# Performance work log

Measured on AMD Instinct MI355X. Metric: run time of the kernel, lower is better.

The kernel has to match this reference:

```python
import jax, jax.numpy as jnp
import numpy as np


def setup_inputs() -> dict:
    key = jax.random.key(0)
    k1, k2, k3, k4 = jax.random.split(key, 4)
    B, C, T, H, W = 2, 64, 8, 48, 48
    C2 = C // 2
    x_in = jax.random.normal(k1, (B, C, T, H, W), dtype=jnp.float32)
    # per-time-slice 1x1 conv weights (theta/phi pairs), kaiming-ish scale
    theta_w = jax.random.normal(k2, (T, C2, C), dtype=jnp.float32) / np.sqrt(C)
    phi_w = jax.random.normal(k3, (T, C2, C), dtype=jnp.float32) / np.sqrt(C)
    out_w = jax.random.normal(k4, (C, C), dtype=jnp.float32) / np.sqrt(C)
    return {"x_in": x_in, "theta_w": theta_w, "phi_w": phi_w, "out_w": out_w}


def reference(x_in, theta_w, phi_w, out_w):
    B, C, T, H, W = x_in.shape
    C2 = theta_w.shape[1]
    P = H * W
    # [B, T, C, P] layout: flatten spatial, move time next to batch
    x = jnp.transpose(x_in, (0, 2, 1, 3, 4)).reshape(B, T, C, P)
    # per-slice 1x1 convs == per-slice channel matmuls with slice-specific weights
    theta = jnp.einsum("toc,btcp->btop", theta_w, x)  # [B,T,C2,P]
    phi = jnp.einsum("toc,btcp->btop", phi_w, x)      # [B,T,C2,P]
    scale = 1.0 / jnp.sqrt(jnp.asarray(C2, dtype=x_in.dtype))
    scores = jnp.einsum("btcp,btcq->btpq", theta, phi) * scale  # [B,T,P,P]
    attn = jax.nn.softmax(scores, axis=-1)
    f = jnp.einsum("btpq,btcq->btcp", attn, x)  # value = raw x, [B,T,C,P]
    # conv_out: 1x1x1 Conv3d (pointwise over channels), then residual
    out = jnp.einsum("oc,btcp->btop", out_w, f)
    out = jnp.transpose(out.reshape(B, T, C, H, W), (0, 2, 1, 3, 4))
    return out + x_in
```

## Files before the change

kernel.cpp:

```cpp
#include <hip/hip_runtime.h>
#include <hip/hip_bf16.h>

#define CC 64
#define TT 8
#define PP 2304
#define C2 32
#define BT 16
#define NKT 36
#define SCALE2 0.25503486f

using h8 = __attribute__((ext_vector_type(8))) _Float16;
using h4 = __attribute__((ext_vector_type(4))) _Float16;
using f4 = __attribute__((ext_vector_type(4))) float;

#if __has_builtin(__builtin_amdgcn_exp2f)
#define EXP2(v) __builtin_amdgcn_exp2f(v)
#else
#define EXP2(v) exp2f(v)
#endif

#define SWIZ_BT(xcd, g) ((xcd) + 8 * ((g) & 1))


__global__ __launch_bounds__(256) void k_prep(
    const float* __restrict__ x, const float* __restrict__ tw,
    const float* __restrict__ pw, _Float16* __restrict__ thf,
    _Float16* __restrict__ rec) {
  const int bt = SWIZ_BT(blockIdx.x, blockIdx.y);
  const int qt = blockIdx.y >> 2;
  const int g = (blockIdx.y >> 1) & 1;
  const int b = bt >> 3, t = bt & 7;
  const int tid = threadIdx.x;
  const int wv = tid >> 6, lane = tid & 63;
  const int quad = lane >> 4, l15 = lane & 15;

  __shared__ __align__(16) float x_s[32][68];
  __shared__ __align__(16) _Float16 th_s[2][16][32];
  __shared__ __align__(16) _Float16 ph_s[2][16][32];

  const size_t xslice = ((size_t)b * CC * TT + t) * PP;
  const int qg0 = qt * 64 + g * 32;
  _Float16* rb = rec + (size_t)(bt * NKT + qt) * 6144;
  const f4 zero = {0.f, 0.f, 0.f, 0.f};

  {
    const int qoff = (tid & 7) * 4;
    const int c0 = tid >> 3;
#pragma unroll
    for (int ppass = 0; ppass < 2; ppass++) {
      const int c = ppass * 32 + c0;
      float4 u = *reinterpret_cast<const float4*>(
          &x[xslice + (size_t)c * (TT * PP) + qg0 + qoff]);
      x_s[qoff + 0][c] = u.x;
      x_s[qoff + 1][c] = u.y;
      x_s[qoff + 2][c] = u.z;
      x_s[qoff + 3][c] = u.w;
    }
  }
  __syncthreads();

  if (wv < 2) {
    h8 bx[2];
#pragma unroll
    for (int ks = 0; ks < 2; ks++) {
      const float* row = &x_s[wv * 16 + l15][ks * 32 + quad * 8];
      float4 u0 = *reinterpret_cast<const float4*>(row);
      float4 u1 = *reinterpret_cast<const float4*>(row + 4);
      bx[ks][0] = (_Float16)u0.x; bx[ks][1] = (_Float16)u0.y;
      bx[ks][2] = (_Float16)u0.z; bx[ks][3] = (_Float16)u0.w;
      bx[ks][4] = (_Float16)u1.x; bx[ks][5] = (_Float16)u1.y;
      bx[ks][6] = (_Float16)u1.z; bx[ks][7] = (_Float16)u1.w;
    }

    const float* twt = tw + t * C2 * CC;
    const float* pwt = pw + t * C2 * CC;
    f4 accT[2] = {zero, zero}, accP[2] = {zero, zero};
#pragma unroll
    for (int mt = 0; mt < 2; mt++)
#pragma unroll
      for (int ks = 0; ks < 2; ks++) {
        const float* wr = twt + (mt * 16 + l15) * CC + ks * 32 + quad * 8;
        const float* pr = pwt + (mt * 16 + l15) * CC + ks * 32 + quad * 8;
        float4 a0 = *reinterpret_cast<const float4*>(wr);
        float4 a1 = *reinterpret_cast<const float4*>(wr + 4);
        float4 p0 = *reinterpret_cast<const float4*>(pr);
        float4 p1 = *reinterpret_cast<const float4*>(pr + 4);
        h8 at = {(_Float16)a0.x, (_Float16)a0.y, (_Float16)a0.z,
                 (_Float16)a0.w, (_Float16)a1.x, (_Float16)a1.y,
                 (_Float16)a1.z, (_Float16)a1.w};
        h8 ap = {(_Float16)p0.x, (_Float16)p0.y, (_Float16)p0.z,
                 (_Float16)p0.w, (_Float16)p1.x, (_Float16)p1.y,
                 (_Float16)p1.z, (_Float16)p1.w};
        accT[mt] = __builtin_amdgcn_mfma_f32_16x16x32_f16(at, bx[ks],
                                                          accT[mt], 0, 0, 0);
        accP[mt] = __builtin_amdgcn_mfma_f32_16x16x32_f16(ap, bx[ks],
                                                          accP[mt], 0, 0, 0);
      }

#pragma unroll
    for (int mt = 0; mt < 2; mt++) {
      h4 tv, pv;
#pragma unroll
      for (int r = 0; r < 4; r++) {
        tv[r] = (_Float16)(accT[mt][r] * SCALE2);
        pv[r] = (_Float16)accP[mt][r];
      }
      *reinterpret_cast<h4*>(&th_s[wv][l15][mt * 16 + quad * 4]) = tv;
      *reinterpret_cast<h4*>(&ph_s[wv][l15][mt * 16 + quad * 4]) = pv;
    }

    h8 tfrag = *reinterpret_cast<const h8*>(&th_s[wv][l15][quad * 8]);
    *reinterpret_cast<h8*>(
        thf + (((size_t)(bt * 144 + qt * 4 + g * 2 + wv)) * 64 + lane) * 8) =
        tfrag;

    h8 pfrag = *reinterpret_cast<const h8*>(&ph_s[wv][l15][quad * 8]);
    *reinterpret_cast<h8*>(rb + (g * 2 + wv) * 512 + lane * 8) = pfrag;
  } else {
    const int w2 = wv - 2;
#pragma unroll
    for (int ct2 = 0; ct2 < 2; ct2++) {
      const int ct = w2 * 2 + ct2;
      h8 v;
#pragma unroll
      for (int j = 0; j < 4; j++) {
        v[j] = (_Float16)x_s[quad * 4 + j][ct * 16 + l15];
        v[4 + j] = (_Float16)x_s[16 + quad * 4 + j][ct * 16 + l15];
      }
      *reinterpret_cast<h8*>(rb + 2048 + (g * 4 + ct) * 512 + lane * 8) = v;
    }
  }
}

__global__ __launch_bounds__(192, 3) void k_attn(
    const float* __restrict__ x, const _Float16* __restrict__ thf,
    const _Float16* __restrict__ rec, const float* __restrict__ ow,
    float* __restrict__ out) {
  const int strip = blockIdx.y >> 1;
  const int bt = SWIZ_BT(blockIdx.x, blockIdx.y);
  const int b = bt >> 3, t = bt & 7;
  const int tid = threadIdx.x;
  const int pf = tid >> 6, lane = tid & 63;
  const int quad = lane >> 4, l15 = lane & 15;

  const h8 bth = *reinterpret_cast<const h8*>(
      thf + (((size_t)bt * 144 + strip * 3 + pf) * 64 + lane) * 8);

  const _Float16* recb = rec + (size_t)bt * NKT * 6144 + lane * 8;

  const f4 zero = {0.f, 0.f, 0.f, 0.f};
  f4 O[4];
#pragma unroll
  for (int ct = 0; ct < 4; ct++) O[ct] = zero;
  float lsum = 0.f;

  h8 hA[6], hB[6];

#define LOADH(BUF, i, gg)                                                    \
  {                                                                          \
    const _Float16* _p = recb + (size_t)(i)*6144;                            \
    BUF[0] = *reinterpret_cast<const h8*>(_p + (2 * (gg)) * 512);            \
    BUF[1] = *reinterpret_cast<const h8*>(_p + (2 * (gg) + 1) * 512);        \
    _Pragma("unroll") for (int c = 0; c < 4; c++)                            \
        BUF[2 + c] =                                                         \
        *reinterpret_cast<const h8*>(_p + 2048 + ((gg)*4 + c) * 512);        \
  }

#define COMPH(BUF)                                                          \
  {                                                                         \
    f4 sA = __builtin_amdgcn_mfma_f32_16x16x32_f16(BUF[0], bth, zero, 0, 0, \
                                                   0);                      \
    f4 sB = __builtin_amdgcn_mfma_f32_16x16x32_f16(BUF[1], bth, zero, 0, 0, \
                                                   0);                      \
    h8 bw;                                                                  \
    _Pragma("unroll") for (int r = 0; r < 4; r++) {                         \
      float w0 = EXP2(sA[r]);                                               \
      float w1 = EXP2(sB[r]);                                               \
      lsum += w0 + w1;                                                      \
      bw[r] = (_Float16)w0;                                                 \
      bw[4 + r] = (_Float16)w1;                                             \
    }                                                                       \
    _Pragma("unroll") for (int ct = 0; ct < 4; ct++)                        \
        O[ct] = __builtin_amdgcn_mfma_f32_16x16x32_f16(BUF[2 + ct], bw,     \
                                                       O[ct], 0, 0, 0);     \
  }

  LOADH(hA, 0, 0);
#pragma unroll 2
  for (int i = 0; i < NKT; i++) {
    LOADH(hB, i, 1);
    COMPH(hA);
    if (i + 1 < NKT) LOADH(hA, i + 1, 0);
    COMPH(hB);
  }
#undef LOADH
#undef COMPH

  lsum += __shfl_xor(lsum, 16);
  lsum += __shfl_xor(lsum, 32);
  const float inv = 1.f / lsum;

  h4 bf[4];
#pragma unroll
  for (int ct = 0; ct < 4; ct++)
#pragma unroll
    for (int r = 0; r < 4; r++) bf[ct][r] = (_Float16)(O[ct][r] * inv);

  f4 D3[4] = {zero, zero, zero, zero};
#pragma unroll
  for (int mt = 0; mt < 4; mt++)
#pragma unroll
    for (int ct = 0; ct < 4; ct++) {
      const float* wrow = ow + (size_t)(mt * 16 + l15) * CC + ct * 16 + quad * 4;
      float4 u = *reinterpret_cast<const float4*>(wrow);
      h4 aw = {(_Float16)u.x, (_Float16)u.y, (_Float16)u.z, (_Float16)u.w};
      D3[mt] = __builtin_amdgcn_mfma_f32_16x16x16f16(aw, bf[ct], D3[mt], 0, 0, 0);
    }

  const int p0 = strip * 48 + pf * 16 + l15;
#pragma unroll
  for (int mt = 0; mt < 4; mt++)
#pragma unroll
    for (int r = 0; r < 4; r++) {
      const int o = mt * 16 + quad * 4 + r;
      const size_t base = ((size_t)(b * CC + o) * TT + t) * PP + p0;
      out[base] = D3[mt][r] + x[base];
    }
}

extern "C" void kernel_launch(void* const* d_in, const int* in_sizes, int n_in,
                              void* d_out, int out_size, void* d_ws,
                              size_t ws_size, hipStream_t stream) {
  (void)in_sizes; (void)n_in; (void)out_size; (void)ws_size;
  const float* x = (const float*)d_in[0];
  const float* tw = (const float*)d_in[1];
  const float* pw = (const float*)d_in[2];
  const float* ow = (const float*)d_in[3];
  float* out = (float*)d_out;

  _Float16* thf = (_Float16*)d_ws;
  _Float16* rec = thf + (size_t)BT * NKT * 4 * 64 * 8;

  k_prep<<<dim3(8, 144), 256, 0, stream>>>(x, tw, pw, thf, rec);
  k_attn<<<dim3(8, 96), 192, 0, stream>>>(x, thf, rec, ow, out);
}
```

Measured before the change: 109.9 us.

## Stage shared key/value tiles in LDS via async global_load_lds ring buffer

Previously each of the three waves in the attention block separately loaded the same phi/x tile from global memory into registers. Now the waves cooperatively copy each tile once into a 4-slot LDS ring with direct global-to-LDS loads, keeping three tiles in flight and synchronising with explicit vmcnt waits and barriers. Each wave then reads its MFMA operands from LDS. The aim is to remove the threefold redundant global/L2 traffic and overlap loads with compute. The cost is 48KB of LDS per block, which may limit occupancy, plus a block-wide barrier on every iteration.

```diff
diff --git a/kernel.cpp b/kernel.cpp
--- a/kernel.cpp
+++ b/kernel.cpp
@@ -21,6 +21,12 @@
 
 #define SWIZ_BT(xcd, g) ((xcd) + 8 * ((g) & 1))
 
+
+__device__ __forceinline__ void gload16(const void* g, void* l) {
+  __builtin_amdgcn_global_load_lds(
+      (const __attribute__((address_space(1))) void*)g,
+      (__attribute__((address_space(3))) void*)l, 16, 0, 0);
+}
 
 __global__ __launch_bounds__(256) void k_prep(
     const float* __restrict__ x, const float* __restrict__ tw,
@@ -143,10 +149,12 @@
   const int pf = tid >> 6, lane = tid & 63;
   const int quad = lane >> 4, l15 = lane & 15;
 
+  __shared__ __align__(16) char smem[4 * 12288];
+
   const h8 bth = *reinterpret_cast<const h8*>(
       thf + (((size_t)bt * 144 + strip * 3 + pf) * 64 + lane) * 8);
 
-  const _Float16* recb = rec + (size_t)bt * NKT * 6144 + lane * 8;
+  const char* recg = (const char*)(rec + (size_t)bt * NKT * 6144);
 
   const f4 zero = {0.f, 0.f, 0.f, 0.f};
   f4 O[4];
@@ -154,47 +162,60 @@
   for (int ct = 0; ct < 4; ct++) O[ct] = zero;
   float lsum = 0.f;
 
-  h8 hA[6], hB[6];
-
-#define LOADH(BUF, i, gg)                                                    \
-  {                                                                          \
-    const _Float16* _p = recb + (size_t)(i)*6144;                            \
-    BUF[0] = *reinterpret_cast<const h8*>(_p + (2 * (gg)) * 512);            \
-    BUF[1] = *reinterpret_cast<const h8*>(_p + (2 * (gg) + 1) * 512);        \
-    _Pragma("unroll") for (int c = 0; c < 4; c++)                            \
-        BUF[2 + c] =                                                         \
-        *reinterpret_cast<const h8*>(_p + 2048 + ((gg)*4 + c) * 512);        \
-  }
-
-#define COMPH(BUF)                                                          \
+#define ISSUE(idx)                                                       \
+  {                                                                      \
+    const char* _g = recg + (size_t)(idx)*12288 + pf * 4096 + lane * 16; \
+    char* _l = smem + ((idx)&3) * 12288 + pf * 4096;                     \
+    _Pragma("unroll") for (int c = 0; c < 4; c++)                        \
+        gload16(_g + c * 1024, _l + c * 1024);                           \
+  }
+
+#define COMPUTE(idx)                                                        \
   {                                                                         \
-    f4 sA = __builtin_amdgcn_mfma_f32_16x16x32_f16(BUF[0], bth, zero, 0, 0, \
-                                                   0);                      \
-    f4 sB = __builtin_amdgcn_mfma_f32_16x16x32_f16(BUF[1], bth, zero, 0, 0, \
-                                                   0);                      \
-    h8 bw;                                                                  \
-    _Pragma("unroll") for (int r = 0; r < 4; r++) {                         \
-      float w0 = EXP2(sA[r]);                                               \
-      float w1 = EXP2(sB[r]);                                               \
-      lsum += w0 + w1;                                                      \
-      bw[r] = (_Float16)w0;                                                 \
-      bw[4 + r] = (_Float16)w1;                                             \
+    const char* _b = smem + ((idx)&3) * 12288;                              \
+    _Pragma("unroll") for (int gg = 0; gg < 2; gg++) {                      \
+      h8 ph0 = *reinterpret_cast<const h8*>(_b + (2 * gg) * 1024 +          \
+                                            lane * 16);                     \
+      h8 ph1 = *reinterpret_cast<const h8*>(_b + (2 * gg + 1) * 1024 +      \
+                                            lane * 16);                     \
+      f4 sA = __builtin_amdgcn_mfma_f32_16x16x32_f16(ph0, bth, zero, 0, 0,  \
+                                                     0);                    \
+      f4 sB = __builtin_amdgcn_mfma_f32_16x16x32_f16(ph1, bth, zero, 0, 0,  \
+                                                     0);                    \
+      h8 bw;                                                                \
+      _Pragma("unroll") for (int r = 0; r < 4; r++) {                       \
+        float w0 = EXP2(sA[r]);                                             \
+        float w1 = EXP2(sB[r]);                                             \
+        lsum += w0 + w1;                                                    \
+        bw[r] = (_Float16)w0;                                               \
+        bw[4 + r] = (_Float16)w1;                                           \
+      }                                                                     \
+      _Pragma("unroll") for (int ct = 0; ct < 4; ct++) {                    \
+        h8 xx = *reinterpret_cast<const h8*>(_b + 4096 +                    \
+                                             (gg * 4 + ct) * 1024 +         \
+                                             lane * 16);                    \
+        O[ct] = __builtin_amdgcn_mfma_f32_16x16x32_f16(xx, bw, O[ct], 0, 0, \
+                                                       0);                  \
+      }                                                                     \
     }                                                                       \
-    _Pragma("unroll") for (int ct = 0; ct < 4; ct++)                        \
-        O[ct] = __builtin_amdgcn_mfma_f32_16x16x32_f16(BUF[2 + ct], bw,     \
-                                                       O[ct], 0, 0, 0);     \
-  }
-
-  LOADH(hA, 0, 0);
-#pragma unroll 2
-  for (int i = 0; i < NKT; i++) {
-    LOADH(hB, i, 1);
-    COMPH(hA);
-    if (i + 1 < NKT) LOADH(hA, i + 1, 0);
-    COMPH(hB);
-  }
-#undef LOADH
-#undef COMPH
+  }
+
+  ISSUE(0);
+  ISSUE(1);
+  ISSUE(2);
+
+#pragma unroll 1
+  for (int i = 0; i < 34; i++) {
+    asm volatile("s_waitcnt vmcnt(8)\n\ts_barrier" ::: "memory");
+    if (i < 33) ISSUE(i + 3);
+    COMPUTE(i);
+  }
+  asm volatile("s_waitcnt vmcnt(4)\n\ts_barrier" ::: "memory");
+  COMPUTE(34);
+  asm volatile("s_waitcnt vmcnt(0)\n\ts_barrier" ::: "memory");
+  COMPUTE(35);
+#undef ISSUE
+#undef COMPUTE
 
   lsum += __shfl_xor(lsum, 16);
   lsum += __shfl_xor(lsum, 32);
```

New measurement: 103.6 us. -5.7%, faster.
